# Kernel tuning notes

Measured on AMD Instinct MI355X. Metric: run time of the kernel, lower is better.

Reference implementation:

```python
import jax, jax.numpy as jnp
import numpy as np

MARGIN = 0.09
SCALE_POS = 2.0
SCALE_NEG = 40.0
EPS = 1e-05
THRESH1 = 0.501
THRESH2 = 0.531


def setup_inputs() -> dict:
    key = jax.random.key(0)
    k1, k2 = jax.random.split(key)
    B, D, N_CLASSES = 4096, 1024, 64
    feats = jax.random.normal(k1, (B, D), dtype=jnp.float32)
    # thresholds in the loss assume cosine-scale similarities -> L2 normalize
    feats = feats / jnp.linalg.norm(feats, axis=1, keepdims=True)
    labels = jax.random.randint(k2, (B,), 0, N_CLASSES, dtype=jnp.int64)
    return {"feats": feats, "labels": labels}


def reference(feats, labels):
    B = feats.shape[0]
    sim = jnp.matmul(feats, feats.T)  # [B, B]
    eq = labels[:, None] == labels[None, :]
    neg_mask = ~eq
    pos_mask = eq & (sim < 1.0 - EPS)  # drops self-similarity (~1)
    # per-row max over negatives; rows with no negatives -> -inf -> no pos survive
    max_neg = jnp.max(jnp.where(neg_mask, sim, -jnp.inf), axis=1)  # [B]
    pos_mask = pos_mask & ((sim - MARGIN) < max_neg[:, None])
    n_pos = jnp.sum(pos_mask, axis=1)
    n_neg = jnp.sum(neg_mask, axis=1)
    pos_sum = jnp.sum(jnp.where(pos_mask, jnp.exp(-SCALE_POS * sim), 0.0), axis=1)
    neg_sum = jnp.sum(jnp.where(neg_mask, jnp.exp(SCALE_NEG * sim), 0.0), axis=1)
    pos_loss = (1.0 / SCALE_POS) * jnp.log(
        (pos_sum + np.exp(-SCALE_POS * THRESH1)) / (n_pos + 1.0))
    neg_loss = (1.0 / SCALE_NEG) * jnp.log(
        (neg_sum + np.exp(SCALE_NEG * THRESH2)) / (n_neg + 1.0))
    per_row = jnp.log(5.33 + jnp.exp(pos_loss + neg_loss))  # [B]
    valid = (n_neg >= 1) & (n_pos >= 1)
    return jnp.sum(jnp.where(valid, per_row, 0.0)) / B
```

## Files before the change

kernel.cpp:

```cpp
#include <hip/hip_runtime.h>
#include <hip/hip_bf16.h>
#include <math.h>

typedef __attribute__((ext_vector_type(8))) short short8;
typedef __attribute__((ext_vector_type(4))) float floatx4;

#define MARGIN_C    0.09f
#define ONE_M_EPS   0.99999f
#define NCLS        64
#define MEMSTRIDE   256

__device__ __forceinline__ unsigned short f2bf(float f) {
    unsigned u = __float_as_uint(f);
    u += 0x7fffu + ((u >> 16) & 1u);
    return (unsigned short)(u >> 16);
}
__device__ __forceinline__ float bf2f(unsigned short v) {
    return __uint_as_float(((unsigned)v) << 16);
}
__device__ __forceinline__ unsigned fkey(float f) {
    unsigned u = __float_as_uint(f);
    return (u >> 31) ? ~u : (u | 0x80000000u);
}
__device__ __forceinline__ float fdec(unsigned k) {
    return __uint_as_float((k >> 31) ? (k & 0x7fffffffu) : ~k);
}

__global__ __launch_bounds__(256) void cvt_build(const float* __restrict__ in,
                                                 unsigned short* __restrict__ out,
                                                 float* __restrict__ statz,
                                                 const int* __restrict__ labels,
                                                 int* __restrict__ members,
                                                 int* __restrict__ classCount,
                                                 int n4, int nz4, int ncvt, int Bn) {
    __shared__ int cnt;
    const int bid = blockIdx.x;
    const int t = threadIdx.x;
    if (bid < ncvt) {
        int i = bid * 256 + t;
        if (i < nz4) ((float4*)statz)[i] = make_float4(0.f, 0.f, 0.f, 0.f);
        if (i >= n4) return;
        float4 v = ((const float4*)in)[i];
        ushort4 o;
        o.x = f2bf(v.x); o.y = f2bf(v.y); o.z = f2bf(v.z); o.w = f2bf(v.w);
        ((ushort4*)out)[i] = o;
    } else {
        const int c = bid - ncvt;
        if (t == 0) cnt = 0;
        __syncthreads();
        for (int j = t; j < Bn; j += 256) {
            if (labels[j] == c) {
                int p = atomicAdd(&cnt, 1);
                if (p < MEMSTRIDE) members[c * MEMSTRIDE + p] = j;
            }
        }
        __syncthreads();
        if (t == 0) classCount[c] = (cnt < MEMSTRIDE) ? cnt : MEMSTRIDE;
    }
}

__global__ __launch_bounds__(256) void gemm_fused(const unsigned short* __restrict__ fb,
                                                  const int* __restrict__ labels,
                                                  float* __restrict__ negsum,
                                                  unsigned* __restrict__ negmax,
                                                  unsigned short* __restrict__ pairsim,
                                                  int Bn, int Dn) {
    __shared__ __align__(16) unsigned short As[2][4096];
    __shared__ __align__(16) unsigned short Bs[2][4096];
    __shared__ int Lrow[128], Lcol[128];

    const int bid = blockIdx.x;
    int by = (int)((sqrtf(8.f * (float)bid + 1.f) - 1.f) * 0.5f);
    while ((by + 1) * (by + 2) / 2 <= bid) by++;
    while (by * (by + 1) / 2 > bid) by--;
    const int bx = bid - by * (by + 1) / 2;

    const int t = threadIdx.x;
    const int wave = t >> 6, lane = t & 63;
    const int wr = wave >> 1, wc = wave & 1;
    const int quad = lane >> 4, m16 = lane & 15;

    if (t < 128) Lrow[t] = labels[by * 128 + t];
    else         Lcol[t - 128] = labels[bx * 128 + (t - 128)];

    const int lr = t >> 2, slot = t & 3, kf = (slot + lr) & 3;
    const unsigned short* gA0 = fb + (size_t)(by * 128 + lr) * Dn + kf * 8;
    const unsigned short* gB0 = fb + (size_t)(bx * 128 + lr) * Dn + kf * 8;
    const unsigned short* gA1 = gA0 + (size_t)64 * Dn;
    const unsigned short* gB1 = gB0 + (size_t)64 * Dn;

    floatx4 acc[4][4];
#pragma unroll
    for (int i = 0; i < 4; i++)
#pragma unroll
        for (int j = 0; j < 4; j++) acc[i][j] = (floatx4){0.f, 0.f, 0.f, 0.f};

    const int fragA = (wr * 64 + m16) * 32 + ((quad - m16) & 3) * 8;
    const int fragB = (wc * 64 + m16) * 32 + ((quad - m16) & 3) * 8;

    const int NS = Dn / 32;
    uint4 ra0 = *(const uint4*)gA0, ra1 = *(const uint4*)gA1;
    uint4 rb0 = *(const uint4*)gB0, rb1 = *(const uint4*)gB1;
    *(uint4*)(&As[0][t * 8]) = ra0;  *(uint4*)(&As[0][2048 + t * 8]) = ra1;
    *(uint4*)(&Bs[0][t * 8]) = rb0;  *(uint4*)(&Bs[0][2048 + t * 8]) = rb1;
    ra0 = *(const uint4*)(gA0 + 32); ra1 = *(const uint4*)(gA1 + 32);
    rb0 = *(const uint4*)(gB0 + 32); rb1 = *(const uint4*)(gB1 + 32);
    __syncthreads();

    for (int s = 0; s < NS; s++) {
        const unsigned short* as_ = As[s & 1];
        const unsigned short* bs_ = Bs[s & 1];
        short8 af[4], bfr[4];
#pragma unroll
        for (int i = 0; i < 4; i++) af[i]  = *(const short8*)(as_ + fragA + i * 512);
#pragma unroll
        for (int i = 0; i < 4; i++) bfr[i] = *(const short8*)(bs_ + fragB + i * 512);
#pragma unroll
        for (int i = 0; i < 4; i++)
#pragma unroll
            for (int j = 0; j < 4; j++)
                acc[i][j] = __builtin_amdgcn_mfma_f32_16x16x32_bf16(af[i], bfr[j], acc[i][j], 0, 0, 0);
        if (s + 1 < NS) {
            __syncthreads();
            unsigned short* aw = As[(s + 1) & 1];
            unsigned short* bw = Bs[(s + 1) & 1];
            *(uint4*)(&aw[t * 8]) = ra0;  *(uint4*)(&aw[2048 + t * 8]) = ra1;
            *(uint4*)(&bw[t * 8]) = rb0;  *(uint4*)(&bw[2048 + t * 8]) = rb1;
            if (s + 2 < NS) {
                const int ko = (s + 2) * 32;
                ra0 = *(const uint4*)(gA0 + ko); ra1 = *(const uint4*)(gA1 + ko);
                rb0 = *(const uint4*)(gB0 + ko); rb1 = *(const uint4*)(gB1 + ko);
            }
            __syncthreads();
        }
    }

    const bool offd = (bx != by);
    int cl[4], gc[4];
#pragma unroll
    for (int j = 0; j < 4; j++) {
        cl[j] = Lcol[wc * 64 + j * 16 + m16];
        gc[j] = bx * 128 + wc * 64 + j * 16 + m16;
    }

    float nsm[4] = {0.f, 0.f, 0.f, 0.f};
    float nmm[4] = {-INFINITY, -INFINITY, -INFINITY, -INFINITY};

#pragma unroll
    for (int i = 0; i < 4; i++) {
#pragma unroll
        for (int r = 0; r < 4; r++) {
            const int rowl = wr * 64 + i * 16 + quad * 4 + r;
            const int rl = Lrow[rowl];
            const int gr = by * 128 + rowl;
            float ns = 0.f, nm = -INFINITY;
#pragma unroll
            for (int j = 0; j < 4; j++) {
                const float s = acc[i][j][r];
                if (cl[j] != rl) {
                    const float e = __expf(40.f * s);
                    ns += e;
                    nm = fmaxf(nm, s);
                    nsm[j] += e;
                    nmm[j] = fmaxf(nmm[j], s);
                } else if ((gr != gc[j]) & (s < ONE_M_EPS)) {
                    const unsigned short v = f2bf(s);
                    pairsim[(size_t)gr * Bn + gc[j]] = v;
                    if (offd) pairsim[(size_t)gc[j] * Bn + gr] = v;
                }
            }
#pragma unroll
            for (int o = 8; o; o >>= 1) {
                ns += __shfl_down(ns, o, 64);
                nm = fmaxf(nm, __shfl_down(nm, o, 64));
            }
            if (m16 == 0) {
                atomicAdd(negsum + gr, ns);
                atomicMax(negmax + gr, fkey(nm));
            }
        }
    }
    if (offd) {
#pragma unroll
        for (int j = 0; j < 4; j++) {
            float v = nsm[j], m = nmm[j];
            v += __shfl_down(v, 16, 64);
            m = fmaxf(m, __shfl_down(m, 16, 64));
            v += __shfl_down(v, 32, 64);
            m = fmaxf(m, __shfl_down(m, 32, 64));
            if (quad == 0) {
                atomicAdd(negsum + gc[j], v);
                atomicMax(negmax + gc[j], fkey(m));
            }
        }
    }
}

__global__ __launch_bounds__(256) void pos_apply(const unsigned short* __restrict__ pairsim,
                                                 const int* __restrict__ labels,
                                                 const int* __restrict__ members,
                                                 const int* __restrict__ classCount,
                                                 const unsigned* __restrict__ negmax,
                                                 float* __restrict__ possum,
                                                 float* __restrict__ nposf, int Bn) {
    const int t = threadIdx.x;
    const int wave = t >> 6, lane = t & 63;
    const int r = blockIdx.x * 4 + wave;
    if (r >= Bn) return;
    const int lab = labels[r];
    const int n = classCount[lab];
    const int base = lab * MEMSTRIDE;
    const float mx = fdec(negmax[r]);
    const unsigned short* prow = pairsim + (size_t)r * Bn;

    float ps = 0.f, pc = 0.f;
    for (int j = lane; j < n; j += 64) {
        const int m = members[base + j];
        if (m != r) {
            const float s = bf2f(prow[m]);
            if ((s - MARGIN_C) < mx) {
                ps += __expf(-2.f * s);
                pc += 1.f;
            }
        }
    }
#pragma unroll
    for (int o = 32; o; o >>= 1) {
        ps += __shfl_down(ps, o, 64);
        pc += __shfl_down(pc, o, 64);
    }
    if (lane == 0) {
        possum[r] = ps;
        nposf[r] = pc;
    }
}

__global__ __launch_bounds__(1024) void finalize(const float* __restrict__ negsum,
                                                 const float* __restrict__ possum,
                                                 const float* __restrict__ nposf,
                                                 const int* __restrict__ labels,
                                                 float* __restrict__ out, int Bn) {
    __shared__ int hist[NCLS];
    __shared__ float red[16];
    const int t = threadIdx.x;
    const int wave = t >> 6, lane = t & 63;
    if (t < NCLS) hist[t] = 0;
    __syncthreads();
    for (int i = t; i < Bn; i += 1024) atomicAdd(&hist[labels[i]], 1);
    __syncthreads();
    float acc = 0.f;
    for (int i = t; i < Bn; i += 1024) {
        const int nneg = Bn - hist[labels[i]];
        const float np = nposf[i];
        if (nneg >= 1 && np >= 0.5f) {
            float pl = 0.5f * logf((possum[i] + expf(-2.f * 0.501f)) / (np + 1.f));
            float nl = (1.f / 40.f) * logf((negsum[i] + expf(40.f * 0.531f)) / ((float)nneg + 1.f));
            acc += logf(5.33f + expf(pl + nl));
        }
    }
#pragma unroll
    for (int o = 32; o; o >>= 1) acc += __shfl_down(acc, o, 64);
    if (lane == 0) red[wave] = acc;
    __syncthreads();
    if (t == 0) {
        float s = 0.f;
        for (int w = 0; w < 16; w++) s += red[w];
        out[0] = s / (float)Bn;
    }
}

extern "C" void kernel_launch(void* const* d_in, const int* in_sizes, int n_in,
                              void* d_out, int out_size, void* d_ws, size_t ws_size,
                              hipStream_t stream) {
    const float* feats = (const float*)d_in[0];
    const int* labels  = (const int*)d_in[1];
    float* out = (float*)d_out;

    const int Bn = in_sizes[1];
    const int Dn = in_sizes[0] / Bn;

    unsigned short* fb = (unsigned short*)d_ws;
    float* stats    = (float*)(fb + (size_t)Bn * Dn);
    float* negsum   = stats;
    unsigned* negmax = (unsigned*)(stats + Bn);
    float* possum   = stats + 2 * Bn;
    float* nposf    = stats + 3 * Bn;
    int* classCount = (int*)(stats + 4 * Bn);
    int* members    = classCount + NCLS;
    unsigned short* pairsim = (unsigned short*)(members + NCLS * MEMSTRIDE);

    const int n4   = (Bn * Dn) / 4;
    const int nz4  = (2 * Bn) / 4;
    const int ncvt = (n4 + 255) / 256;
    cvt_build<<<ncvt + NCLS, 256, 0, stream>>>(feats, fb, stats, labels,
                                               members, classCount, n4, nz4, ncvt, Bn);

    const int nt = Bn / 128;
    const int ntri = nt * (nt + 1) / 2;
    gemm_fused<<<ntri, 256, 0, stream>>>(fb, labels, negsum, negmax, pairsim, Bn, Dn);

    pos_apply<<<(Bn + 3) / 4, 256, 0, stream>>>(pairsim, labels, members, classCount,
                                                negmax, possum, nposf, Bn);

    finalize<<<1, 1024, 0, stream>>>(negsum, possum, nposf, labels, out, Bn);
}
```

Before: 125.0 us.

## Deepen GEMM K-step to 64, share diagonal tile loads, fuse pos and finalize kernels

The GEMM now stages a 64-wide K slice per iteration with an 8-chunk XOR swizzle, which halves the number of barrier-separated steps. Diagonal tiles load only the A operand and reuse it as B. The positive-pair pass and the single-block finalize are merged into one kernel that computes per-row loss and accumulates it into the output with an atomic add, so one launch goes away. The cost is doubled LDS use per block, which may lower occupancy, and an atomic float sum whose order is nondeterministic.

Measured after the change: 188.7 us. 1.51x slower.

```diff
diff --git a/kernel.cpp b/kernel.cpp
--- a/kernel.cpp
+++ b/kernel.cpp
@@ -32,12 +32,14 @@
                                                  const int* __restrict__ labels,
                                                  int* __restrict__ members,
                                                  int* __restrict__ classCount,
+                                                 float* __restrict__ loss_out,
                                                  int n4, int nz4, int ncvt, int Bn) {
     __shared__ int cnt;
     const int bid = blockIdx.x;
     const int t = threadIdx.x;
     if (bid < ncvt) {
         int i = bid * 256 + t;
+        if (bid == 0 && t == 0) loss_out[0] = 0.0f;
         if (i < nz4) ((float4*)statz)[i] = make_float4(0.f, 0.f, 0.f, 0.f);
         if (i >= n4) return;
         float4 v = ((const float4*)in)[i];
@@ -65,8 +67,8 @@
                                                   unsigned* __restrict__ negmax,
                                                   unsigned short* __restrict__ pairsim,
                                                   int Bn, int Dn) {
-    __shared__ __align__(16) unsigned short As[2][4096];
-    __shared__ __align__(16) unsigned short Bs[2][4096];
+    __shared__ __align__(16) unsigned short As[2][8192];
+    __shared__ __align__(16) unsigned short Bs[2][8192];
     __shared__ int Lrow[128], Lcol[128];
 
     const int bid = blockIdx.x;
@@ -74,6 +76,7 @@
     while ((by + 1) * (by + 2) / 2 <= bid) by++;
     while (by * (by + 1) / 2 > bid) by--;
     const int bx = bid - by * (by + 1) / 2;
+    const bool diag = (bx == by);
 
     const int t = threadIdx.x;
     const int wave = t >> 6, lane = t & 63;
@@ -83,11 +86,18 @@
     if (t < 128) Lrow[t] = labels[by * 128 + t];
     else         Lcol[t - 128] = labels[bx * 128 + (t - 128)];
 
-    const int lr = t >> 2, slot = t & 3, kf = (slot + lr) & 3;
-    const unsigned short* gA0 = fb + (size_t)(by * 128 + lr) * Dn + kf * 8;
-    const unsigned short* gB0 = fb + (size_t)(bx * 128 + lr) * Dn + kf * 8;
-    const unsigned short* gA1 = gA0 + (size_t)64 * Dn;
-    const unsigned short* gB1 = gB0 + (size_t)64 * Dn;
+    const unsigned short* gA[4];
+    const unsigned short* gB[4];
+    int lofs[4];
+#pragma unroll
+    for (int q = 0; q < 4; q++) {
+        const int g = q * 256 + t;
+        const int row = g >> 3, s = g & 7;
+        const int gch = (s + row) & 7;
+        gA[q] = fb + (size_t)(by * 128 + row) * Dn + gch * 8;
+        gB[q] = fb + (size_t)(bx * 128 + row) * Dn + gch * 8;
+        lofs[q] = g * 8;
+    }
 
     floatx4 acc[4][4];
 #pragma unroll
@@ -95,47 +105,80 @@
 #pragma unroll
         for (int j = 0; j < 4; j++) acc[i][j] = (floatx4){0.f, 0.f, 0.f, 0.f};
 
-    const int fragA = (wr * 64 + m16) * 32 + ((quad - m16) & 3) * 8;
-    const int fragB = (wc * 64 + m16) * 32 + ((quad - m16) & 3) * 8;
-
-    const int NS = Dn / 32;
-    uint4 ra0 = *(const uint4*)gA0, ra1 = *(const uint4*)gA1;
-    uint4 rb0 = *(const uint4*)gB0, rb1 = *(const uint4*)gB1;
-    *(uint4*)(&As[0][t * 8]) = ra0;  *(uint4*)(&As[0][2048 + t * 8]) = ra1;
-    *(uint4*)(&Bs[0][t * 8]) = rb0;  *(uint4*)(&Bs[0][2048 + t * 8]) = rb1;
-    ra0 = *(const uint4*)(gA0 + 32); ra1 = *(const uint4*)(gA1 + 32);
-    rb0 = *(const uint4*)(gB0 + 32); rb1 = *(const uint4*)(gB1 + 32);
+    const int fragRowA = (wr * 64 + m16) * 64;
+    const int fragRowB = (wc * 64 + m16) * 64;
+    const int slotK0 = ((quad)-m16) & 7;
+    const int slotK1 = ((4 + quad) - m16) & 7;
+
+    const int NS = Dn / 64;
+    uint4 ra[4], rb[4];
+#pragma unroll
+    for (int q = 0; q < 4; q++) ra[q] = *(const uint4*)gA[q];
+    if (!diag) {
+#pragma unroll
+        for (int q = 0; q < 4; q++) rb[q] = *(const uint4*)gB[q];
+    }
+#pragma unroll
+    for (int q = 0; q < 4; q++) *(uint4*)(&As[0][lofs[q]]) = ra[q];
+    if (!diag) {
+#pragma unroll
+        for (int q = 0; q < 4; q++) *(uint4*)(&Bs[0][lofs[q]]) = rb[q];
+    }
+#pragma unroll
+    for (int q = 0; q < 4; q++) ra[q] = *(const uint4*)(gA[q] + 64);
+    if (!diag) {
+#pragma unroll
+        for (int q = 0; q < 4; q++) rb[q] = *(const uint4*)(gB[q] + 64);
+    }
     __syncthreads();
 
     for (int s = 0; s < NS; s++) {
         const unsigned short* as_ = As[s & 1];
-        const unsigned short* bs_ = Bs[s & 1];
+        const unsigned short* bs_ = diag ? as_ : Bs[s & 1];
         short8 af[4], bfr[4];
 #pragma unroll
-        for (int i = 0; i < 4; i++) af[i]  = *(const short8*)(as_ + fragA + i * 512);
-#pragma unroll
-        for (int i = 0; i < 4; i++) bfr[i] = *(const short8*)(bs_ + fragB + i * 512);
+        for (int i = 0; i < 4; i++) af[i]  = *(const short8*)(as_ + fragRowA + i * 1024 + slotK0 * 8);
+#pragma unroll
+        for (int i = 0; i < 4; i++) bfr[i] = *(const short8*)(bs_ + fragRowB + i * 1024 + slotK0 * 8);
 #pragma unroll
         for (int i = 0; i < 4; i++)
 #pragma unroll
             for (int j = 0; j < 4; j++)
                 acc[i][j] = __builtin_amdgcn_mfma_f32_16x16x32_bf16(af[i], bfr[j], acc[i][j], 0, 0, 0);
+#pragma unroll
+        for (int i = 0; i < 4; i++) af[i]  = *(const short8*)(as_ + fragRowA + i * 1024 + slotK1 * 8);
+#pragma unroll
+        for (int i = 0; i < 4; i++) bfr[i] = *(const short8*)(bs_ + fragRowB + i * 1024 + slotK1 * 8);
+#pragma unroll
+        for (int i = 0; i < 4; i++)
+#pragma unroll
+            for (int j = 0; j < 4; j++)
+                acc[i][j] = __builtin_amdgcn_mfma_f32_16x16x32_bf16(af[i], bfr[j], acc[i][j], 0, 0, 0);
+
         if (s + 1 < NS) {
             __syncthreads();
             unsigned short* aw = As[(s + 1) & 1];
-            unsigned short* bw = Bs[(s + 1) & 1];
-            *(uint4*)(&aw[t * 8]) = ra0;  *(uint4*)(&aw[2048 + t * 8]) = ra1;
-            *(uint4*)(&bw[t * 8]) = rb0;  *(uint4*)(&bw[2048 + t * 8]) = rb1;
+#pragma unroll
+            for (int q = 0; q < 4; q++) *(uint4*)(&aw[lofs[q]]) = ra[q];
+            if (!diag) {
+                unsigned short* bw = Bs[(s + 1) & 1];
+#pragma unroll
+                for (int q = 0; q < 4; q++) *(uint4*)(&bw[lofs[q]]) = rb[q];
+            }
             if (s + 2 < NS) {
-                const int ko = (s + 2) * 32;
-                ra0 = *(const uint4*)(gA0 + ko); ra1 = *(const uint4*)(gA1 + ko);
-                rb0 = *(const uint4*)(gB0 + ko); rb1 = *(const uint4*)(gB1 + ko);
+                const int ko = (s + 2) * 64;
+#pragma unroll
+                for (int q = 0; q < 4; q++) ra[q] = *(const uint4*)(gA[q] + ko);
+                if (!diag) {
+#pragma unroll
+                    for (int q = 0; q < 4; q++) rb[q] = *(const uint4*)(gB[q] + ko);
+                }
             }
             __syncthreads();
         }
     }
 
-    const bool offd = (bx != by);
+    const bool offd = !diag;
     int cl[4], gc[4];
 #pragma unroll
     for (int j = 0; j < 4; j++) {
@@ -196,76 +239,56 @@
     }
 }
 
-__global__ __launch_bounds__(256) void pos_apply(const unsigned short* __restrict__ pairsim,
+__global__ __launch_bounds__(256) void pos_final(const unsigned short* __restrict__ pairsim,
                                                  const int* __restrict__ labels,
                                                  const int* __restrict__ members,
                                                  const int* __restrict__ classCount,
                                                  const unsigned* __restrict__ negmax,
-                                                 float* __restrict__ possum,
-                                                 float* __restrict__ nposf, int Bn) {
+                                                 const float* __restrict__ negsum,
+                                                 float* __restrict__ out, int Bn) {
+    __shared__ float part[4];
     const int t = threadIdx.x;
     const int wave = t >> 6, lane = t & 63;
-    const int r = blockIdx.x * 4 + wave;
-    if (r >= Bn) return;
-    const int lab = labels[r];
-    const int n = classCount[lab];
-    const int base = lab * MEMSTRIDE;
-    const float mx = fdec(negmax[r]);
-    const unsigned short* prow = pairsim + (size_t)r * Bn;
-
-    float ps = 0.f, pc = 0.f;
-    for (int j = lane; j < n; j += 64) {
-        const int m = members[base + j];
-        if (m != r) {
-            const float s = bf2f(prow[m]);
-            if ((s - MARGIN_C) < mx) {
-                ps += __expf(-2.f * s);
-                pc += 1.f;
-            }
-        }
-    }
-#pragma unroll
-    for (int o = 32; o; o >>= 1) {
-        ps += __shfl_down(ps, o, 64);
-        pc += __shfl_down(pc, o, 64);
-    }
-    if (lane == 0) {
-        possum[r] = ps;
-        nposf[r] = pc;
-    }
-}
-
-__global__ __launch_bounds__(1024) void finalize(const float* __restrict__ negsum,
-                                                 const float* __restrict__ possum,
-                                                 const float* __restrict__ nposf,
-                                                 const int* __restrict__ labels,
-                                                 float* __restrict__ out, int Bn) {
-    __shared__ int hist[NCLS];
-    __shared__ float red[16];
-    const int t = threadIdx.x;
-    const int wave = t >> 6, lane = t & 63;
-    if (t < NCLS) hist[t] = 0;
-    __syncthreads();
-    for (int i = t; i < Bn; i += 1024) atomicAdd(&hist[labels[i]], 1);
-    __syncthreads();
-    float acc = 0.f;
-    for (int i = t; i < Bn; i += 1024) {
-        const int nneg = Bn - hist[labels[i]];
-        const float np = nposf[i];
-        if (nneg >= 1 && np >= 0.5f) {
-            float pl = 0.5f * logf((possum[i] + expf(-2.f * 0.501f)) / (np + 1.f));
-            float nl = (1.f / 40.f) * logf((negsum[i] + expf(40.f * 0.531f)) / ((float)nneg + 1.f));
-            acc += logf(5.33f + expf(pl + nl));
-        }
-    }
-#pragma unroll
-    for (int o = 32; o; o >>= 1) acc += __shfl_down(acc, o, 64);
-    if (lane == 0) red[wave] = acc;
+    float wacc = 0.f;
+#pragma unroll
+    for (int rr = 0; rr < 4; rr++) {
+        const int r = blockIdx.x * 16 + wave * 4 + rr;
+        if (r >= Bn) break;
+        const int lab = labels[r];
+        const int n = classCount[lab];
+        const int base = lab * MEMSTRIDE;
+        const float mx = fdec(negmax[r]);
+        const unsigned short* prow = pairsim + (size_t)r * Bn;
+
+        float ps = 0.f, pc = 0.f;
+        for (int j = lane; j < n; j += 64) {
+            const int m = members[base + j];
+            if (m != r) {
+                const float s = bf2f(prow[m]);
+                if ((s - MARGIN_C) < mx) {
+                    ps += __expf(-2.f * s);
+                    pc += 1.f;
+                }
+            }
+        }
+#pragma unroll
+        for (int o = 32; o; o >>= 1) {
+            ps += __shfl_down(ps, o, 64);
+            pc += __shfl_down(pc, o, 64);
+        }
+        if (lane == 0) {
+            const int nneg = Bn - n;
+            if (nneg >= 1 && pc >= 0.5f) {
+                float pl = 0.5f * logf((ps + expf(-2.f * 0.501f)) / (pc + 1.f));
+                float nl = (1.f / 40.f) * logf((negsum[r] + expf(40.f * 0.531f)) / ((float)nneg + 1.f));
+                wacc += logf(5.33f + expf(pl + nl));
+            }
+        }
+    }
+    if (lane == 0) part[wave] = wacc;
     __syncthreads();
     if (t == 0) {
-        float s = 0.f;
-        for (int w = 0; w < 16; w++) s += red[w];
-        out[0] = s / (float)Bn;
+        atomicAdd(out, (part[0] + part[1] + part[2] + part[3]) / (float)Bn);
     }
 }
 
@@ -283,9 +306,7 @@
     float* stats    = (float*)(fb + (size_t)Bn * Dn);
     float* negsum   = stats;
     unsigned* negmax = (unsigned*)(stats + Bn);
-    float* possum   = stats + 2 * Bn;
-    float* nposf    = stats + 3 * Bn;
-    int* classCount = (int*)(stats + 4 * Bn);
+    int* classCount = (int*)(stats + 2 * Bn);
     int* members    = classCount + NCLS;
     unsigned short* pairsim = (unsigned short*)(members + NCLS * MEMSTRIDE);
 
@@ -293,14 +314,13 @@
     const int nz4  = (2 * Bn) / 4;
     const int ncvt = (n4 + 255) / 256;
     cvt_build<<<ncvt + NCLS, 256, 0, stream>>>(feats, fb, stats, labels,
-                                               members, classCount, n4, nz4, ncvt, Bn);
+                                               members, classCount, out,
+                                               n4, nz4, ncvt, Bn);
 
     const int nt = Bn / 128;
     const int ntri = nt * (nt + 1) / 2;
     gemm_fused<<<ntri, 256, 0, stream>>>(fb, labels, negsum, negmax, pairsim, Bn, Dn);
 
-    pos_apply<<<(Bn + 3) / 4, 256, 0, stream>>>(pairsim, labels, members, classCount,
-                                                negmax, possum, nposf, Bn);
-
-    finalize<<<1, 1024, 0, stream>>>(negsum, possum, nposf, labels, out, Bn);
-}
+    pos_final<<<(Bn + 15) / 16, 256, 0, stream>>>(pairsim, labels, members, classCount,
+                                                  negmax, negsum, out, Bn);
+}
```
